# Performance work log

Measured on AMD Instinct MI355X. Metric: run time of the kernel, lower is better.

## Reference

```python
import jax, jax.numpy as jnp
import numpy as np

B, T, D = 2, 4096, 512
H = 8  # heads; head_dim = D // H = 64


def setup_inputs() -> dict:
    key = jax.random.key(0)
    ks = jax.random.split(key, 8)
    s = 0.02
    return {
        "queries": jax.random.normal(ks[0], (B, T, D), jnp.float32),
        "keys": jax.random.normal(ks[1], (B, T, D), jnp.float32),
        "values": jax.random.normal(ks[2], (B, T, D), jnp.float32),
        "Wq": jax.random.normal(ks[3], (D, D), jnp.float32) * s,
        "Wk": jax.random.normal(ks[4], (D, D), jnp.float32) * s,
        "Wv": jax.random.normal(ks[5], (D, D), jnp.float32) * s,
        "Wo": jax.random.normal(ks[6], (D, D), jnp.float32) * s,
        "bo": jnp.zeros((D,), jnp.float32),
    }


def reference(queries, keys, values, Wq, Wk, Wv, Wo, bo):
    # pad_dim = 0 for in_dim=512, n_heads=8, so no padding needed.
    Bq, Tq, _ = queries.shape
    Ts = keys.shape[1]
    hd = D // H
    # torch Linear: x @ W.T
    q = (queries @ Wq.T).reshape(Bq, Tq, H, hd).transpose(0, 2, 1, 3)  # [B,H,T,hd]
    k = (keys @ Wk.T).reshape(Bq, Ts, H, hd).transpose(0, 2, 1, 3)
    v = (values @ Wv.T).reshape(Bq, Ts, H, hd).transpose(0, 2, 1, 3)
    attn = jnp.einsum("bhtd,bhsd->bhts", q, k) / np.sqrt(hd).astype(np.float32)
    attn = jax.nn.softmax(attn, axis=-1)  # [B,H,T,Ts]
    z = jnp.einsum("bhts,bhsd->bhtd", attn, v)
    z = z.transpose(0, 2, 1, 3).reshape(Bq, Tq, D)
    out = z @ Wo.T + bo
    return (out, attn)
```

## Files before the change

kernel.cpp:

```cpp
#include <hip/hip_runtime.h>

typedef __attribute__((ext_vector_type(8))) short bf16x8;
typedef __attribute__((ext_vector_type(8))) unsigned short u16x8;
typedef __attribute__((ext_vector_type(4))) float f32x4;
typedef __attribute__((ext_vector_type(2))) unsigned uint2v;
typedef __attribute__((ext_vector_type(4))) unsigned uint4v;

#define DEVINL __device__ __forceinline__

constexpr int TB = 2;
constexpr int TT = 4096;
constexpr int TD = 512;
constexpr int TH = 8;
constexpr int THD = 64;
constexpr int TM = TB * TT;

DEVINL unsigned short f2b(float f) {
  unsigned u = __builtin_bit_cast(unsigned, f);
  u += 0x7FFFu + ((u >> 16) & 1u);
  return (unsigned short)(u >> 16);
}

DEVINL unsigned cvtpk(float lo, float hi) {
  unsigned r;
  asm("v_cvt_pk_bf16_f32 %0, %1, %2" : "=v"(r) : "v"(lo), "v"(hi));
  return r;
}

DEVINL void lgkm_barrier() {
  asm volatile("s_waitcnt lgkmcnt(0)" ::: "memory");
  __builtin_amdgcn_s_barrier();
  __builtin_amdgcn_sched_barrier(0);
}

__global__ __launch_bounds__(256, 2)
void proj_qkv(const float* __restrict__ Xq, const float* __restrict__ Xk,
              const float* __restrict__ Xv, const float* __restrict__ Wq,
              const float* __restrict__ Wk, const float* __restrict__ Wv,
              unsigned short* __restrict__ qb, unsigned short* __restrict__ kb,
              unsigned short* __restrict__ vt)
{
  constexpr int K = TD, N = TD;
  __shared__ unsigned short As[128][72];
  __shared__ unsigned short Bs[128][72];

  const int z = blockIdx.z;
  const float* X = (z == 0) ? Xq : (z == 1) ? Xk : Xv;
  const float* W = (z == 0) ? Wq : (z == 1) ? Wk : Wv;
  unsigned short* Yb = (z == 0) ? qb : (z == 1) ? kb : vt;
  const bool TR = (z == 2);

  const int t    = threadIdx.x;
  const int lane = t & 63, w = t >> 6;
  const int fr = lane & 15, fq = lane >> 4;
  const int wr = (w >> 1) * 64, wc = (w & 1) * 64;
  const int bm = blockIdx.x * 128, bn = blockIdx.y * 128;
  const int srow = t >> 1;
  const int skh  = (t & 1) * 32;

  f32x4 acc[4][4];
  #pragma unroll
  for (int i = 0; i < 4; ++i)
    #pragma unroll
    for (int j = 0; j < 4; ++j)
      acc[i][j] = f32x4{0.f, 0.f, 0.f, 0.f};

  for (int k0 = 0; k0 < K; k0 += 64) {
    const float* srcA = X + (size_t)(bm + srow) * K + k0 + skh;
    const float* srcB = W + (size_t)(bn + srow) * K + k0 + skh;
    #pragma unroll
    for (int i = 0; i < 4; ++i) {
      float4 a0 = ((const float4*)srcA)[2 * i];
      float4 a1 = ((const float4*)srcA)[2 * i + 1];
      u16x8 oa = {f2b(a0.x), f2b(a0.y), f2b(a0.z), f2b(a0.w),
                  f2b(a1.x), f2b(a1.y), f2b(a1.z), f2b(a1.w)};
      *(u16x8*)&As[srow][skh + i * 8] = oa;
      float4 b0 = ((const float4*)srcB)[2 * i];
      float4 b1 = ((const float4*)srcB)[2 * i + 1];
      u16x8 ob = {f2b(b0.x), f2b(b0.y), f2b(b0.z), f2b(b0.w),
                  f2b(b1.x), f2b(b1.y), f2b(b1.z), f2b(b1.w)};
      *(u16x8*)&Bs[srow][skh + i * 8] = ob;
    }
    __syncthreads();
    #pragma unroll
    for (int kk = 0; kk < 2; ++kk) {
      bf16x8 af[4], bfv[4];
      #pragma unroll
      for (int i = 0; i < 4; ++i)
        af[i] = *(const bf16x8*)&As[wr + i * 16 + fr][kk * 32 + fq * 8];
      #pragma unroll
      for (int j = 0; j < 4; ++j)
        bfv[j] = *(const bf16x8*)&Bs[wc + j * 16 + fr][kk * 32 + fq * 8];
      if (TR) {
        #pragma unroll
        for (int i = 0; i < 4; ++i)
          #pragma unroll
          for (int j = 0; j < 4; ++j)
            acc[i][j] = __builtin_amdgcn_mfma_f32_16x16x32_bf16(bfv[i], af[j], acc[i][j], 0, 0, 0);
      } else {
        #pragma unroll
        for (int i = 0; i < 4; ++i)
          #pragma unroll
          for (int j = 0; j < 4; ++j)
            acc[i][j] = __builtin_amdgcn_mfma_f32_16x16x32_bf16(af[i], bfv[j], acc[i][j], 0, 0, 0);
      }
    }
    __syncthreads();
  }

  if (TR) {
    #pragma unroll
    for (int i = 0; i < 4; ++i)
      #pragma unroll
      for (int j = 0; j < 4; ++j)
        #pragma unroll
        for (int ii = 0; ii < 4; ++ii) {
          const int Nidx = bn + wc + i * 16 + fq * 4 + ii;
          const int Midx = bm + wr + j * 16 + fr;
          const int h = Nidx >> 6, dd = Nidx & (THD - 1);
          const int b = Midx >> 12, tt = Midx & (TT - 1);
          Yb[((size_t)(b * TH + h) * THD + dd) * TT + tt] = f2b(acc[i][j][ii]);
        }
  } else {
    #pragma unroll
    for (int i = 0; i < 4; ++i)
      #pragma unroll
      for (int j = 0; j < 4; ++j)
        #pragma unroll
        for (int ii = 0; ii < 4; ++ii) {
          const int gm = bm + wr + i * 16 + fq * 4 + ii;
          const int gn = bn + wc + j * 16 + fr;
          Yb[(size_t)gm * N + gn] = f2b(acc[i][j][ii]);
        }
  }
}

__global__ __launch_bounds__(256, 2)
void gemm_final(const float* __restrict__ X, const float* __restrict__ W,
                float* __restrict__ Yf, const float* __restrict__ bias)
{
  constexpr int K = TD, N = TD;
  __shared__ unsigned short As[128][72];
  __shared__ unsigned short Bs[128][72];

  const int t    = threadIdx.x;
  const int lane = t & 63, w = t >> 6;
  const int fr = lane & 15, fq = lane >> 4;
  const int wr = (w >> 1) * 64, wc = (w & 1) * 64;
  const int bm = blockIdx.x * 128, bn = blockIdx.y * 128;
  const int srow = t >> 1;
  const int skh  = (t & 1) * 32;

  f32x4 acc[4][4];
  #pragma unroll
  for (int i = 0; i < 4; ++i)
    #pragma unroll
    for (int j = 0; j < 4; ++j)
      acc[i][j] = f32x4{0.f, 0.f, 0.f, 0.f};

  for (int k0 = 0; k0 < K; k0 += 64) {
    const float* srcA = X + (size_t)(bm + srow) * K + k0 + skh;
    const float* srcB = W + (size_t)(bn + srow) * K + k0 + skh;
    #pragma unroll
    for (int i = 0; i < 4; ++i) {
      float4 a0 = ((const float4*)srcA)[2 * i];
      float4 a1 = ((const float4*)srcA)[2 * i + 1];
      u16x8 oa = {f2b(a0.x), f2b(a0.y), f2b(a0.z), f2b(a0.w),
                  f2b(a1.x), f2b(a1.y), f2b(a1.z), f2b(a1.w)};
      *(u16x8*)&As[srow][skh + i * 8] = oa;
      float4 b0 = ((const float4*)srcB)[2 * i];
      float4 b1 = ((const float4*)srcB)[2 * i + 1];
      u16x8 ob = {f2b(b0.x), f2b(b0.y), f2b(b0.z), f2b(b0.w),
                  f2b(b1.x), f2b(b1.y), f2b(b1.z), f2b(b1.w)};
      *(u16x8*)&Bs[srow][skh + i * 8] = ob;
    }
    __syncthreads();
    #pragma unroll
    for (int kk = 0; kk < 2; ++kk) {
      bf16x8 af[4], bfv[4];
      #pragma unroll
      for (int i = 0; i < 4; ++i)
        af[i] = *(const bf16x8*)&As[wr + i * 16 + fr][kk * 32 + fq * 8];
      #pragma unroll
      for (int j = 0; j < 4; ++j)
        bfv[j] = *(const bf16x8*)&Bs[wc + j * 16 + fr][kk * 32 + fq * 8];
      #pragma unroll
      for (int i = 0; i < 4; ++i)
        #pragma unroll
        for (int j = 0; j < 4; ++j)
          acc[i][j] = __builtin_amdgcn_mfma_f32_16x16x32_bf16(af[i], bfv[j], acc[i][j], 0, 0, 0);
    }
    __syncthreads();
  }

  #pragma unroll
  for (int i = 0; i < 4; ++i)
    #pragma unroll
    for (int j = 0; j < 4; ++j)
      #pragma unroll
      for (int ii = 0; ii < 4; ++ii) {
        const int gm = bm + wr + i * 16 + fq * 4 + ii;
        const int gn = bn + wc + j * 16 + fr;
        Yf[(size_t)gm * N + gn] = acc[i][j][ii] + bias[gn];
      }
}

__global__ __launch_bounds__(256, 4)
void attn_fused(const unsigned short* __restrict__ Qb,
                const unsigned short* __restrict__ Kb,
                const unsigned short* __restrict__ VTg,
                float* __restrict__ attnO, float* __restrict__ Z)
{
  __shared__ unsigned short Ks[2][32][72];
  __shared__ unsigned short VTs[2][64][40];

  const int t    = threadIdx.x;
  const int lane = t & 63, w = t >> 6;
  const int fr = lane & 15, fq = lane >> 4;

  const int d  = blockIdx.x;
  const int bh = 2 * (d & 7) + ((d >> 3) & 1);
  const int q0 = (d >> 4) * 64;
  const int b  = bh >> 3, h = bh & 7;

  const size_t rowKV  = ((size_t)(b * TT)) * TD + h * THD;
  const size_t vtBase = (size_t)bh * THD * TT;

  const int trK = t >> 3, tcK = (t & 7) * 8;
  const int trV = t >> 2, tcV = (t & 3) * 8;

  auto loadK = [&](int kv0, u16x8& r) {
    r = *(const u16x8*)(Kb + rowKV + (size_t)(kv0 + trK) * TD + tcK);
  };
  auto loadVT = [&](int kv0, u16x8& r) {
    r = *(const u16x8*)(VTg + vtBase + (size_t)trV * TT + kv0 + tcV);
  };
  auto writeK  = [&](int buf, const u16x8& r) { *(u16x8*)&Ks[buf][trK][tcK]  = r; };
  auto writeVT = [&](int buf, const u16x8& r) { *(u16x8*)&VTs[buf][trV][tcV] = r; };

  const unsigned short* qsrc = Qb + ((size_t)(b * TT + q0 + w * 16 + fr)) * TD + h * THD;
  bf16x8 aq[2];
  aq[0] = *(const bf16x8*)(qsrc + fq * 8);
  aq[1] = *(const bf16x8*)(qsrc + 32 + fq * 8);

  constexpr int KVB = 32;
  constexpr int NT = TT / KVB;
  constexpr float K2 = 0.18033688011112042f;

  u16x8 kr, vr;
  loadK(0, kr);
  loadVT(0, vr);
  writeK(0, kr);
  writeVT(0, vr);
  lgkm_barrier();

  float lsum = 0.f;
  f32x4 accz[4];
  #pragma unroll
  for (int n = 0; n < 4; ++n) accz[n] = f32x4{0.f, 0.f, 0.f, 0.f};

  for (int j = 0; j < NT; ++j) {
    const int cur = j & 1;
    if (j + 1 < NT) {
      loadK((j + 1) * KVB, kr);
      loadVT((j + 1) * KVB, vr);
    }
    f32x4 sv[2];
    __builtin_amdgcn_s_setprio(1);
    #pragma unroll
    for (int n = 0; n < 2; ++n) {
      f32x4 s = f32x4{0.f, 0.f, 0.f, 0.f};
      #pragma unroll
      for (int kk = 0; kk < 2; ++kk) {
        bf16x8 ak = *(const bf16x8*)&Ks[cur][n * 16 + fr][kk * 32 + fq * 8];
        s = __builtin_amdgcn_mfma_f32_16x16x32_bf16(ak, aq[kk], s, 0, 0, 0);
      }
      sv[n] = s;
    }
    __builtin_amdgcn_s_setprio(0);
    float p[2][4];
    #pragma unroll
    for (int n = 0; n < 2; ++n)
      #pragma unroll
      for (int i = 0; i < 4; ++i) {
        p[n][i] = __builtin_amdgcn_exp2f(sv[n][i] * K2);
        lsum += p[n][i];
      }
    uint4v pav = {cvtpk(p[0][0], p[0][1]), cvtpk(p[0][2], p[0][3]),
                  cvtpk(p[1][0], p[1][1]), cvtpk(p[1][2], p[1][3])};
    bf16x8 ap = __builtin_bit_cast(bf16x8, pav);
    __builtin_amdgcn_s_setprio(1);
    #pragma unroll
    for (int df = 0; df < 4; ++df) {
      uint2v lo = *(const uint2v*)&VTs[cur][df * 16 + fr][fq * 4];
      uint2v hi = *(const uint2v*)&VTs[cur][df * 16 + fr][16 + fq * 4];
      uint4v bvv = {lo[0], lo[1], hi[0], hi[1]};
      accz[df] = __builtin_amdgcn_mfma_f32_16x16x32_bf16(
          ap, __builtin_bit_cast(bf16x8, bvv), accz[df], 0, 0, 0);
    }
    __builtin_amdgcn_s_setprio(0);
    if (j + 1 < NT) {
      writeK(cur ^ 1, kr);
      writeVT(cur ^ 1, vr);
    }
    lgkm_barrier();
  }

  lsum += __shfl_xor(lsum, 16, 64);
  lsum += __shfl_xor(lsum, 32, 64);

  float rls[4];
  #pragma unroll
  for (int i = 0; i < 4; ++i)
    rls[i] = 1.0f / __shfl(lsum, fq * 4 + i, 64);
  const size_t zbase = ((size_t)(b * TT + q0 + w * 16 + fq * 4)) * TD + h * THD + fr;
  #pragma unroll
  for (int df = 0; df < 4; ++df)
    #pragma unroll
    for (int i = 0; i < 4; ++i)
      Z[zbase + (size_t)i * TD + df * 16] = accz[df][i] * rls[i];

  const float l2i = -__log2f(lsum);
  loadK(0, kr);
  writeK(0, kr);
  lgkm_barrier();

  float* arow = attnO + ((size_t)bh * TT + q0 + w * 16 + fr) * TT + fq * 4;

  for (int j = 0; j < NT; ++j) {
    const int cur = j & 1;
    if (j + 1 < NT) loadK((j + 1) * KVB, kr);
    f32x4 sv[2];
    __builtin_amdgcn_s_setprio(1);
    #pragma unroll
    for (int n = 0; n < 2; ++n) {
      f32x4 s = f32x4{0.f, 0.f, 0.f, 0.f};
      #pragma unroll
      for (int kk = 0; kk < 2; ++kk) {
        bf16x8 ak = *(const bf16x8*)&Ks[cur][n * 16 + fr][kk * 32 + fq * 8];
        s = __builtin_amdgcn_mfma_f32_16x16x32_bf16(ak, aq[kk], s, 0, 0, 0);
      }
      sv[n] = s;
    }
    __builtin_amdgcn_s_setprio(0);
    #pragma unroll
    for (int n = 0; n < 2; ++n) {
      f32x4 pv4 = {__builtin_amdgcn_exp2f(fmaf(sv[n][0], K2, l2i)),
                   __builtin_amdgcn_exp2f(fmaf(sv[n][1], K2, l2i)),
                   __builtin_amdgcn_exp2f(fmaf(sv[n][2], K2, l2i)),
                   __builtin_amdgcn_exp2f(fmaf(sv[n][3], K2, l2i))};
      *(f32x4*)(arow + j * KVB + n * 16) = pv4;
    }
    if (j + 1 < NT) writeK(cur ^ 1, kr);
    lgkm_barrier();
  }
}

extern "C" void kernel_launch(void* const* d_in, const int* in_sizes, int n_in,
                              void* d_out, int out_size, void* d_ws, size_t ws_size,
                              hipStream_t stream) {
  const float* queries = (const float*)d_in[0];
  const float* keys    = (const float*)d_in[1];
  const float* values  = (const float*)d_in[2];
  const float* Wq = (const float*)d_in[3];
  const float* Wk = (const float*)d_in[4];
  const float* Wv = (const float*)d_in[5];
  const float* Wo = (const float*)d_in[6];
  const float* bo = (const float*)d_in[7];

  float* out  = (float*)d_out;
  float* attn = out + (size_t)TM * TD;

  unsigned short* qb = (unsigned short*)d_ws;
  unsigned short* kb = qb + (size_t)TM * TD;
  unsigned short* vt = kb + (size_t)TM * TD;
  float*          zf = (float*)(vt + (size_t)TM * TD);

  proj_qkv<<<dim3(TM / 128, TD / 128, 3), 256, 0, stream>>>(
      queries, keys, values, Wq, Wk, Wv, qb, kb, vt);

  attn_fused<<<dim3(1024), 256, 0, stream>>>(qb, kb, vt, attn, zf);

  gemm_final<<<dim3(TM / 128, TD / 128), 256, 0, stream>>>(zf, Wo, out, bo);
}
```

Measured before the change: 521.8 us.

## Give each wave private K buffers and stagger its attn write pass

In the second pass that recomputes scores and writes normalized attention probabilities, each wave now loads its own copy of the K tile into a per-wave LDS region. This removes the block-wide barrier on every iteration. Each wave also starts at a rotated KV tile offset (phase), so different waves and blocks spread their attn stores across memory instead of writing the same columns together. The cost is four times the K global loads and a larger LDS footprint (36 KB), which can lower occupancy. There is also no explicit wait between a wave's LDS write and its next read, so correctness depends on wave-level ordering.

New measurement: 501.7 us. 1.04x faster.

```diff
diff --git a/kernel.cpp b/kernel.cpp
--- a/kernel.cpp
+++ b/kernel.cpp
@@ -211,8 +211,10 @@
                 const unsigned short* __restrict__ VTg,
                 float* __restrict__ attnO, float* __restrict__ Z)
 {
-  __shared__ unsigned short Ks[2][32][72];
-  __shared__ unsigned short VTs[2][64][40];
+  __shared__ __align__(16) char smem_[36864];
+  auto Ks  = (unsigned short (*)[32][72])smem_;
+  auto VTs = (unsigned short (*)[64][40])(smem_ + 9216);
+  auto KsW = (unsigned short (*)[2][32][72])smem_;
 
   const int t    = threadIdx.x;
   const int lane = t & 63, w = t >> 6;
@@ -321,15 +323,32 @@
       Z[zbase + (size_t)i * TD + df * 16] = accz[df][i] * rls[i];
 
   const float l2i = -__log2f(lsum);
-  loadK(0, kr);
-  writeK(0, kr);
-  lgkm_barrier();
+  __syncthreads();
+
+  const int phase = (37 * d + 32 * w) & (NT - 1);
+  const int prow = lane >> 3, pcol = (lane & 7) * 8;
+  u16x8 kr4[4];
+  auto loadKW = [&](int kvt) {
+    #pragma unroll
+    for (int i = 0; i < 4; ++i)
+      kr4[i] = *(const u16x8*)(Kb + rowKV +
+                 (size_t)(kvt * KVB + i * 8 + prow) * TD + pcol);
+  };
+  auto writeKW = [&](int buf) {
+    #pragma unroll
+    for (int i = 0; i < 4; ++i)
+      *(u16x8*)&KsW[w][buf][i * 8 + prow][pcol] = kr4[i];
+  };
+
+  loadKW(phase);
+  writeKW(0);
 
   float* arow = attnO + ((size_t)bh * TT + q0 + w * 16 + fr) * TT + fq * 4;
 
-  for (int j = 0; j < NT; ++j) {
-    const int cur = j & 1;
-    if (j + 1 < NT) loadK((j + 1) * KVB, kr);
+  for (int jj = 0; jj < NT; ++jj) {
+    const int cur = jj & 1;
+    const int j = (jj + phase) & (NT - 1);
+    if (jj + 1 < NT) loadKW((jj + 1 + phase) & (NT - 1));
     f32x4 sv[2];
     __builtin_amdgcn_s_setprio(1);
     #pragma unroll
@@ -337,7 +356,7 @@
       f32x4 s = f32x4{0.f, 0.f, 0.f, 0.f};
       #pragma unroll
       for (int kk = 0; kk < 2; ++kk) {
-        bf16x8 ak = *(const bf16x8*)&Ks[cur][n * 16 + fr][kk * 32 + fq * 8];
+        bf16x8 ak = *(const bf16x8*)&KsW[w][cur][n * 16 + fr][kk * 32 + fq * 8];
         s = __builtin_amdgcn_mfma_f32_16x16x32_bf16(ak, aq[kk], s, 0, 0, 0);
       }
       sv[n] = s;
@@ -351,8 +370,7 @@
                    __builtin_amdgcn_exp2f(fmaf(sv[n][3], K2, l2i))};
       *(f32x4*)(arow + j * KVB + n * 16) = pv4;
     }
-    if (j + 1 < NT) writeK(cur ^ 1, kr);
-    lgkm_barrier();
+    if (jj + 1 < NT) writeKW(cur ^ 1);
   }
 }
 
```

## Split fused attention into two kernels with per-wave staggered K tiles

Applied to the files above, without the earlier changes.

Splits the fused attention kernel into a first pass that computes the row sums and Z, writing per-row log-normalizers to workspace, and a second pass that recomputes the scores and writes the normalized attention matrix. The first pass now prefetches K/V two tiles ahead. In the second pass each wave loads its own K tiles into a private shared buffer with no block barriers, and starts at a phase-shifted tile to spread the large attention writes and K reads across memory. This adds a kernel launch and an extra Q load, and uses more shared memory in pass 2, which may lower occupancy.

Measured after the change: 490.7 us (median of 2 runs). -6.0%, faster.

```diff
diff --git a/kernel.cpp b/kernel.cpp
--- a/kernel.cpp
+++ b/kernel.cpp
@@ -206,10 +206,10 @@
 }
 
 __global__ __launch_bounds__(256, 4)
-void attn_fused(const unsigned short* __restrict__ Qb,
+void attn_pass1(const unsigned short* __restrict__ Qb,
                 const unsigned short* __restrict__ Kb,
                 const unsigned short* __restrict__ VTg,
-                float* __restrict__ attnO, float* __restrict__ Z)
+                float* __restrict__ Z, float* __restrict__ l2iW)
 {
   __shared__ unsigned short Ks[2][32][72];
   __shared__ unsigned short VTs[2][64][40];
@@ -247,67 +247,76 @@
   constexpr int NT = TT / KVB;
   constexpr float K2 = 0.18033688011112042f;
 
-  u16x8 kr, vr;
-  loadK(0, kr);
-  loadVT(0, vr);
-  writeK(0, kr);
-  writeVT(0, vr);
-  lgkm_barrier();
+  u16x8 kA, vA, kB, vB;
+  {
+    u16x8 k0, v0;
+    loadK(0, k0); loadVT(0, v0);
+    writeK(0, k0); writeVT(0, v0);
+    loadK(KVB, kB); loadVT(KVB, vB);
+    lgkm_barrier();
+  }
 
   float lsum = 0.f;
   f32x4 accz[4];
   #pragma unroll
   for (int n = 0; n < 4; ++n) accz[n] = f32x4{0.f, 0.f, 0.f, 0.f};
 
-  for (int j = 0; j < NT; ++j) {
-    const int cur = j & 1;
-    if (j + 1 < NT) {
-      loadK((j + 1) * KVB, kr);
-      loadVT((j + 1) * KVB, vr);
+  for (int jp = 0; jp < NT / 2; ++jp) {
+    #pragma unroll
+    for (int half = 0; half < 2; ++half) {
+      const int j = jp * 2 + half;
+      const int cur = j & 1;
+      if (j + 2 < NT) {
+        if (half == 0) { loadK((j + 2) * KVB, kA); loadVT((j + 2) * KVB, vA); }
+        else           { loadK((j + 2) * KVB, kB); loadVT((j + 2) * KVB, vB); }
+      }
+      f32x4 sv[2];
+      __builtin_amdgcn_s_setprio(1);
+      #pragma unroll
+      for (int n = 0; n < 2; ++n) {
+        f32x4 s = f32x4{0.f, 0.f, 0.f, 0.f};
+        #pragma unroll
+        for (int kk = 0; kk < 2; ++kk) {
+          bf16x8 ak = *(const bf16x8*)&Ks[cur][n * 16 + fr][kk * 32 + fq * 8];
+          s = __builtin_amdgcn_mfma_f32_16x16x32_bf16(ak, aq[kk], s, 0, 0, 0);
+        }
+        sv[n] = s;
+      }
+      __builtin_amdgcn_s_setprio(0);
+      float p[2][4];
+      #pragma unroll
+      for (int n = 0; n < 2; ++n)
+        #pragma unroll
+        for (int i = 0; i < 4; ++i) {
+          p[n][i] = __builtin_amdgcn_exp2f(sv[n][i] * K2);
+          lsum += p[n][i];
+        }
+      uint4v pav = {cvtpk(p[0][0], p[0][1]), cvtpk(p[0][2], p[0][3]),
+                    cvtpk(p[1][0], p[1][1]), cvtpk(p[1][2], p[1][3])};
+      bf16x8 ap = __builtin_bit_cast(bf16x8, pav);
+      __builtin_amdgcn_s_setprio(1);
+      #pragma unroll
+      for (int df = 0; df < 4; ++df) {
+        uint2v lo = *(const uint2v*)&VTs[cur][df * 16 + fr][fq * 4];
+        uint2v hi = *(const uint2v*)&VTs[cur][df * 16 + fr][16 + fq * 4];
+        uint4v bvv = {lo[0], lo[1], hi[0], hi[1]};
+        accz[df] = __builtin_amdgcn_mfma_f32_16x16x32_bf16(
+            ap, __builtin_bit_cast(bf16x8, bvv), accz[df], 0, 0, 0);
+      }
+      __builtin_amdgcn_s_setprio(0);
+      if (j + 1 < NT) {
+        if (half == 0) { writeK(cur ^ 1, kB); writeVT(cur ^ 1, vB); }
+        else           { writeK(cur ^ 1, kA); writeVT(cur ^ 1, vA); }
+      }
+      lgkm_barrier();
     }
-    f32x4 sv[2];
-    __builtin_amdgcn_s_setprio(1);
-    #pragma unroll
-    for (int n = 0; n < 2; ++n) {
-      f32x4 s = f32x4{0.f, 0.f, 0.f, 0.f};
-      #pragma unroll
-      for (int kk = 0; kk < 2; ++kk) {
-        bf16x8 ak = *(const bf16x8*)&Ks[cur][n * 16 + fr][kk * 32 + fq * 8];
-        s = __builtin_amdgcn_mfma_f32_16x16x32_bf16(ak, aq[kk], s, 0, 0, 0);
-      }
-      sv[n] = s;
-    }
-    __builtin_amdgcn_s_setprio(0);
-    float p[2][4];
-    #pragma unroll
-    for (int n = 0; n < 2; ++n)
-      #pragma unroll
-      for (int i = 0; i < 4; ++i) {
-        p[n][i] = __builtin_amdgcn_exp2f(sv[n][i] * K2);
-        lsum += p[n][i];
-      }
-    uint4v pav = {cvtpk(p[0][0], p[0][1]), cvtpk(p[0][2], p[0][3]),
-                  cvtpk(p[1][0], p[1][1]), cvtpk(p[1][2], p[1][3])};
-    bf16x8 ap = __builtin_bit_cast(bf16x8, pav);
-    __builtin_amdgcn_s_setprio(1);
-    #pragma unroll
-    for (int df = 0; df < 4; ++df) {
-      uint2v lo = *(const uint2v*)&VTs[cur][df * 16 + fr][fq * 4];
-      uint2v hi = *(const uint2v*)&VTs[cur][df * 16 + fr][16 + fq * 4];
-      uint4v bvv = {lo[0], lo[1], hi[0], hi[1]};
-      accz[df] = __builtin_amdgcn_mfma_f32_16x16x32_bf16(
-          ap, __builtin_bit_cast(bf16x8, bvv), accz[df], 0, 0, 0);
-    }
-    __builtin_amdgcn_s_setprio(0);
-    if (j + 1 < NT) {
-      writeK(cur ^ 1, kr);
-      writeVT(cur ^ 1, vr);
-    }
-    lgkm_barrier();
   }
 
   lsum += __shfl_xor(lsum, 16, 64);
   lsum += __shfl_xor(lsum, 32, 64);
+
+  if (fq == 0)
+    l2iW[(size_t)bh * TT + q0 + w * 16 + fr] = -__log2f(lsum);
 
   float rls[4];
   #pragma unroll
@@ -319,41 +328,97 @@
     #pragma unroll
     for (int i = 0; i < 4; ++i)
       Z[zbase + (size_t)i * TD + df * 16] = accz[df][i] * rls[i];
-
-  const float l2i = -__log2f(lsum);
-  loadK(0, kr);
-  writeK(0, kr);
-  lgkm_barrier();
+}
+
+__global__ __launch_bounds__(256, 4)
+void attn_pass2(const unsigned short* __restrict__ Qb,
+                const unsigned short* __restrict__ Kb,
+                const float* __restrict__ l2iW,
+                float* __restrict__ attnO)
+{
+  __shared__ unsigned short KsW[4][2][32][72];
+
+  const int t    = threadIdx.x;
+  const int lane = t & 63, w = t >> 6;
+  const int fr = lane & 15, fq = lane >> 4;
+
+  const int d  = blockIdx.x;
+  const int bh = 2 * (d & 7) + ((d >> 3) & 1);
+  const int q0 = (d >> 4) * 64;
+  const int b  = bh >> 3, h = bh & 7;
+
+  const size_t rowKV = ((size_t)(b * TT)) * TD + h * THD;
+
+  const unsigned short* qsrc = Qb + ((size_t)(b * TT + q0 + w * 16 + fr)) * TD + h * THD;
+  bf16x8 aq[2];
+  aq[0] = *(const bf16x8*)(qsrc + fq * 8);
+  aq[1] = *(const bf16x8*)(qsrc + 32 + fq * 8);
+
+  const float l2i = l2iW[(size_t)bh * TT + q0 + w * 16 + fr];
+
+  constexpr int KVB = 32;
+  constexpr int NT = TT / KVB;
+  constexpr float K2 = 0.18033688011112042f;
+
+  const int phase = (37 * d + 32 * w) & (NT - 1);
+  const int prow = lane >> 3, pcol = (lane & 7) * 8;
+
+  u16x8 sA[4], sB[4];
+  auto loadKW = [&](int kvt, u16x8* s) {
+    #pragma unroll
+    for (int i = 0; i < 4; ++i)
+      s[i] = *(const u16x8*)(Kb + rowKV +
+               (size_t)(kvt * KVB + i * 8 + prow) * TD + pcol);
+  };
+  auto writeKW = [&](int buf, const u16x8* s) {
+    #pragma unroll
+    for (int i = 0; i < 4; ++i)
+      *(u16x8*)&KsW[w][buf][i * 8 + prow][pcol] = s[i];
+  };
+  auto PH = [&](int jj) { return (jj + phase) & (NT - 1); };
 
   float* arow = attnO + ((size_t)bh * TT + q0 + w * 16 + fr) * TT + fq * 4;
 
-  for (int j = 0; j < NT; ++j) {
-    const int cur = j & 1;
-    if (j + 1 < NT) loadK((j + 1) * KVB, kr);
-    f32x4 sv[2];
-    __builtin_amdgcn_s_setprio(1);
-    #pragma unroll
-    for (int n = 0; n < 2; ++n) {
-      f32x4 s = f32x4{0.f, 0.f, 0.f, 0.f};
-      #pragma unroll
-      for (int kk = 0; kk < 2; ++kk) {
-        bf16x8 ak = *(const bf16x8*)&Ks[cur][n * 16 + fr][kk * 32 + fq * 8];
-        s = __builtin_amdgcn_mfma_f32_16x16x32_bf16(ak, aq[kk], s, 0, 0, 0);
-      }
-      sv[n] = s;
-    }
-    __builtin_amdgcn_s_setprio(0);
-    #pragma unroll
-    for (int n = 0; n < 2; ++n) {
-      f32x4 pv4 = {__builtin_amdgcn_exp2f(fmaf(sv[n][0], K2, l2i)),
-                   __builtin_amdgcn_exp2f(fmaf(sv[n][1], K2, l2i)),
-                   __builtin_amdgcn_exp2f(fmaf(sv[n][2], K2, l2i)),
-                   __builtin_amdgcn_exp2f(fmaf(sv[n][3], K2, l2i))};
-      *(f32x4*)(arow + j * KVB + n * 16) = pv4;
-    }
-    if (j + 1 < NT) writeK(cur ^ 1, kr);
-    lgkm_barrier();
-  }
+#define P2_COMPUTE(JJ, BUF)                                                    \
+  {                                                                            \
+    const int j = PH(JJ);                                                      \
+    f32x4 sv[2];                                                               \
+    __builtin_amdgcn_s_setprio(1);                                             \
+    _Pragma("unroll")                                                          \
+    for (int n = 0; n < 2; ++n) {                                              \
+      f32x4 s = f32x4{0.f, 0.f, 0.f, 0.f};                                     \
+      _Pragma("unroll")                                                        \
+      for (int kk = 0; kk < 2; ++kk) {                                         \
+        bf16x8 ak = *(const bf16x8*)&KsW[w][(BUF)][n * 16 + fr][kk * 32 + fq * 8]; \
+        s = __builtin_amdgcn_mfma_f32_16x16x32_bf16(ak, aq[kk], s, 0, 0, 0);   \
+      }                                                                        \
+      sv[n] = s;                                                               \
+    }                                                                          \
+    __builtin_amdgcn_s_setprio(0);                                             \
+    _Pragma("unroll")                                                          \
+    for (int n = 0; n < 2; ++n) {                                              \
+      f32x4 pv4 = {__builtin_amdgcn_exp2f(fmaf(sv[n][0], K2, l2i)),            \
+                   __builtin_amdgcn_exp2f(fmaf(sv[n][1], K2, l2i)),            \
+                   __builtin_amdgcn_exp2f(fmaf(sv[n][2], K2, l2i)),            \
+                   __builtin_amdgcn_exp2f(fmaf(sv[n][3], K2, l2i))};           \
+      *(f32x4*)(arow + j * KVB + n * 16) = pv4;                                \
+    }                                                                          \
+  }
+
+  loadKW(PH(0), sA);
+  writeKW(0, sA);
+  loadKW(PH(1), sB);
+
+  for (int jp = 0; jp < NT / 2; ++jp) {
+    const int jj0 = 2 * jp;
+    if (jj0 + 2 < NT) loadKW(PH(jj0 + 2), sA);
+    P2_COMPUTE(jj0, 0)
+    writeKW(1, sB);
+    if (jj0 + 3 < NT) loadKW(PH(jj0 + 3), sB);
+    P2_COMPUTE(jj0 + 1, 1)
+    if (jj0 + 2 < NT) writeKW(0, sA);
+  }
+#undef P2_COMPUTE
 }
 
 extern "C" void kernel_launch(void* const* d_in, const int* in_sizes, int n_in,
@@ -375,11 +440,14 @@
   unsigned short* kb = qb + (size_t)TM * TD;
   unsigned short* vt = kb + (size_t)TM * TD;
   float*          zf = (float*)(vt + (size_t)TM * TD);
+  float*          l2iW = zf + (size_t)TM * TD;
 
   proj_qkv<<<dim3(TM / 128, TD / 128, 3), 256, 0, stream>>>(
       queries, keys, values, Wq, Wk, Wv, qb, kb, vt);
 
-  attn_fused<<<dim3(1024), 256, 0, stream>>>(qb, kb, vt, attn, zf);
+  attn_pass1<<<dim3(1024), 256, 0, stream>>>(qb, kb, vt, zf, l2iW);
+
+  attn_pass2<<<dim3(1024), 256, 0, stream>>>(qb, kb, l2iW, attn);
 
   gemm_final<<<dim3(TM / 128, TD / 128), 256, 0, stream>>>(zf, Wo, out, bo);
 }
```
